# Kernel tuning notes

Hardware: AMD Instinct MI355X
Metric: run time of the kernel (lower is better)

## Reference

```python
import jax, jax.numpy as jnp
import numpy as np

EPS = 1e-5  # BatchNorm2d default eps


def _median_pool3x3(x):
    # x: [B,1,H,W]; 3x3 kernel, stride 1, pad 1 (zero padding, matching F.unfold).
    B, C, H, W = x.shape
    xp = jnp.pad(x, ((0, 0), (0, 0), (1, 1), (1, 1)))
    # Stack the 9 shifted views -> [B,C,H,W,9]; torch.median returns the LOWER
    # median, i.e. sorted index (9-1)//2 = 4 for 9 elements.
    patches = jnp.stack([xp[:, :, i:i + H, j:j + W]
                         for i in range(3) for j in range(3)], axis=-1)
    return jnp.sort(patches, axis=-1)[..., 4]


def _batchnorm_train(x, w, b):
    # BatchNorm2d(1) in training mode: biased variance over (B,H,W) per channel.
    m = jnp.mean(x, axis=(0, 2, 3), keepdims=True)
    v = jnp.mean((x - m) ** 2, axis=(0, 2, 3), keepdims=True)
    return (x - m) * jax.lax.rsqrt(v + EPS) * w.reshape(1, -1, 1, 1) + b.reshape(1, -1, 1, 1)


def _shift_grid_sample(x, xshift, yshift):
    # Faithful to Shift.forward + F.grid_sample(mode='bilinear',
    # padding_mode='zeros', align_corners=False).
    B, C, Nv, Nh = x.shape
    yreg = (jnp.arange(Nv, dtype=x.dtype) - yshift) * 10.0  # [Nv]
    xreg = (jnp.arange(Nh, dtype=x.dtype) - xshift) * 10.0  # [Nh]
    Hv, Wv = Nv * 10.0, Nh * 10.0  # virtual upsampled size used for normalization
    gy = 2.0 * yreg / Hv - 1.0
    gx = 2.0 * xreg / Wv - 1.0
    # unnormalize (align_corners=False): pix = ((g+1)*size - 1)/2
    iy = ((gy + 1.0) * Nv - 1.0) * 0.5  # [Nv]
    ix = ((gx + 1.0) * Nh - 1.0) * 0.5  # [Nh]
    IY, IX = jnp.meshgrid(iy, ix, indexing='ij')  # [Nv,Nh] each

    x0 = jnp.floor(IX); x1 = x0 + 1.0
    y0 = jnp.floor(IY); y1 = y0 + 1.0
    wx1 = IX - x0; wx0 = 1.0 - wx1
    wy1 = IY - y0; wy0 = 1.0 - wy1

    def gather(yc, xc):
        valid = ((yc >= 0) & (yc < Nv) & (xc >= 0) & (xc < Nh)).astype(x.dtype)
        yi = jnp.clip(yc, 0, Nv - 1).astype(jnp.int32)
        xi = jnp.clip(xc, 0, Nh - 1).astype(jnp.int32)
        return x[:, :, yi, xi] * valid  # [B,C,Nv,Nh], zeros outside

    return (gather(y0, x0) * (wy0 * wx0) + gather(y0, x1) * (wy0 * wx1)
            + gather(y1, x0) * (wy1 * wx0) + gather(y1, x1) * (wy1 * wx1))


def setup_inputs() -> dict:
    key = jax.random.key(0)
    ks = jax.random.split(key, 4)
    B, Nv, Nh = 131072, 8, 16
    num_classes, channels = 8, Nv * Nh
    x = jax.random.normal(ks[0], (B, 1, Nv, Nh), dtype=jnp.float32)
    bn_weight = jnp.ones((1,), dtype=jnp.float32)
    bn_bias = jnp.zeros((1,), dtype=jnp.float32)
    xshift = jax.random.uniform(ks[1], (1,), dtype=jnp.float32)
    yshift = jax.random.uniform(ks[2], (1,), dtype=jnp.float32)
    fc_w = jax.random.normal(ks[3], (num_classes, channels), dtype=jnp.float32) / np.sqrt(channels)
    fc_b = jnp.zeros((num_classes,), dtype=jnp.float32)
    return {"x": x, "bn_weight": bn_weight, "bn_bias": bn_bias,
            "xshift": xshift, "yshift": yshift, "fc_w": fc_w, "fc_b": fc_b}


def reference(x, bn_weight, bn_bias, xshift, yshift, fc_w, fc_b):
    h = _median_pool3x3(x)
    h = _batchnorm_train(h, bn_weight, bn_bias)
    h = _shift_grid_sample(h, xshift, yshift)
    h = h.reshape(h.shape[0], -1)  # [B, Nv*Nh]
    return h @ fc_w.T + fc_b  # [B, num_classes]
```

## Files before the change

kernel.cpp:

```cpp
#include <hip/hip_runtime.h>
#include <math.h>

#define NBLK 4096


__device__ __forceinline__ float med3f(float a, float b, float c) {
  return __builtin_amdgcn_fmed3f(a, b, c);
}
__device__ __forceinline__ float min3f(float a, float b, float c) { return fminf(fminf(a, b), c); }
__device__ __forceinline__ float max3f(float a, float b, float c) { return fmaxf(fmaxf(a, b), c); }

__device__ __forceinline__ void fold_weights(int p, const float* __restrict__ fc_w,
                                             float sx, float sy, float* __restrict__ w8) {
  const int y = p >> 4, x = p & 15;
  const int dY = (sy > 1.0f) ? 2 : 1;
  const int dX = (sx > 1.0f) ? 2 : 1;
  const float wy1 = (float)dY - sy, wy0 = 1.0f - wy1;
  const float wx1 = (float)dX - sx, wx0 = 1.0f - wx1;
  const int   iys[2] = { y + dY - 1, y + dY };
  const float wys[2] = { wy1, wy0 };
  const int   jxs[2] = { x + dX - 1, x + dX };
  const float wxs[2] = { wx1, wx0 };
  #pragma unroll
  for (int c = 0; c < 8; ++c) {
    float acc = 0.0f;
    #pragma unroll
    for (int a = 0; a < 2; ++a) {
      if (iys[a] < 0 || iys[a] >= 8) continue;
      #pragma unroll
      for (int b = 0; b < 2; ++b) {
        if (jxs[b] < 0 || jxs[b] >= 16) continue;
        acc += wys[a] * wxs[b] * fc_w[c * 128 + iys[a] * 16 + jxs[b]];
      }
    }
    w8[c] = acc;
  }
}

__global__ __launch_bounds__(256, 2) void k_main(const float* __restrict__ x,
                                                 const float* __restrict__ fcw,
                                                 const float* __restrict__ xs,
                                                 const float* __restrict__ ys,
                                                 float* __restrict__ out,
                                                 float* __restrict__ partial) {
  __shared__ float wlds[8][16][8];
  __shared__ float sred[8];
  const int tid = threadIdx.x;
  const int w = tid >> 6, l = tid & 63;
  const int row = l & 7;
  const int g   = w * 8 + (l >> 3);
  const int img = blockIdx.x * 32 + g;
  const float* __restrict__ xi = x + (size_t)img * 128;

  float mid[16];
  #pragma unroll
  for (int q = 0; q < 4; ++q)
    *(float4*)&mid[q * 4] = *(const float4*)&xi[row * 16 + q * 4];

  const float sx = xs[0] + 0.5f, sy = ys[0] + 0.5f;
  if (tid < 128) {
    float w8[8];
    fold_weights(tid, fcw, sx, sy, w8);
    const int r = tid >> 4, j = tid & 15;
    #pragma unroll
    for (int c = 0; c < 8; ++c) wlds[r][j ^ r][c] = w8[c];
  }
  __syncthreads();

  float up[16], dn[16];
  #pragma unroll
  for (int k = 0; k < 16; ++k) {
    const float u = __shfl_up(mid[k], 1, 16);
    const float d = __shfl_down(mid[k], 1, 16);
    up[k] = (row == 0) ? 0.0f : u;
    dn[k] = (row == 7) ? 0.0f : d;
  }

  #pragma unroll
  for (int k = 0; k < 16; ++k) {
    const float a = up[k], b = mid[k], d = dn[k];
    up[k]  = min3f(a, b, d);
    mid[k] = med3f(a, b, d);
    dn[k]  = max3f(a, b, d);
  }

  float acc[8];
  #pragma unroll
  for (int c = 0; c < 8; ++c) acc[c] = 0.0f;
  float ssum = 0.0f, ssq = 0.0f;

  #pragma unroll
  for (int j = 0; j < 16; ++j) {
    const float mx  = max3f((j == 0)  ? 0.0f : up[j - 1],  up[j],
                            (j == 15) ? 0.0f : up[j + 1]);
    const float md  = med3f((j == 0)  ? 0.0f : mid[j - 1], mid[j],
                            (j == 15) ? 0.0f : mid[j + 1]);
    const float mn  = min3f((j == 0)  ? 0.0f : dn[j - 1],  dn[j],
                            (j == 15) ? 0.0f : dn[j + 1]);
    const float med = med3f(mx, md, mn);
    ssum += med;
    ssq = fmaf(med, med, ssq);
    const float* wp = &wlds[row][j ^ row][0];
    const float4 w0 = *(const float4*)&wp[0];
    const float4 w1 = *(const float4*)&wp[4];
    acc[0] = fmaf(med, w0.x, acc[0]);
    acc[1] = fmaf(med, w0.y, acc[1]);
    acc[2] = fmaf(med, w0.z, acc[2]);
    acc[3] = fmaf(med, w0.w, acc[3]);
    acc[4] = fmaf(med, w1.x, acc[4]);
    acc[5] = fmaf(med, w1.y, acc[5]);
    acc[6] = fmaf(med, w1.z, acc[6]);
    acc[7] = fmaf(med, w1.w, acc[7]);
  }

  const bool b4 = (l & 4) != 0;
  float r4[4];
  #pragma unroll
  for (int j = 0; j < 4; ++j) {
    const float send = b4 ? acc[j] : acc[4 + j];
    const float keep = b4 ? acc[4 + j] : acc[j];
    r4[j] = keep + __shfl_xor(send, 4, 64);
  }
  const bool b2 = (l & 2) != 0;
  float r2[2];
  #pragma unroll
  for (int j = 0; j < 2; ++j) {
    const float send = b2 ? r4[j] : r4[2 + j];
    const float keep = b2 ? r4[2 + j] : r4[j];
    r2[j] = keep + __shfl_xor(send, 2, 64);
  }
  const bool b1 = (l & 1) != 0;
  {
    const float send = b1 ? r2[0] : r2[1];
    const float keep = b1 ? r2[1] : r2[0];
    const float r = keep + __shfl_xor(send, 1, 64);
    out[(size_t)img * 8 + (l & 7)] = r;
  }

  #pragma unroll
  for (int off = 32; off; off >>= 1) {
    ssum += __shfl_xor(ssum, off, 64);
    ssq  += __shfl_xor(ssq,  off, 64);
  }
  if (l == 0) { sred[w] = ssum; sred[4 + w] = ssq; }
  __syncthreads();
  if (tid == 0) partial[2 * blockIdx.x]     = (sred[0] + sred[1]) + (sred[2] + sred[3]);
  if (tid == 1) partial[2 * blockIdx.x + 1] = (sred[4] + sred[5]) + (sred[6] + sred[7]);
}

__global__ __launch_bounds__(256) void k_scale(float* __restrict__ out,
                                               const float* __restrict__ partial,
                                               const float* __restrict__ fcw,
                                               const float* __restrict__ xs,
                                               const float* __restrict__ ys,
                                               const float* __restrict__ fcb,
                                               const float* __restrict__ bnw,
                                               const float* __restrict__ bnb) {
  __shared__ float sred[8];
  __shared__ float wred[4][8];
  __shared__ float fin[2];
  const int tid = threadIdx.x;
  const int w = tid >> 6, l = tid & 63;

  float s = 0.0f, q = 0.0f;
  #pragma unroll
  for (int k = 0; k < 16; ++k) {
    const int idx = tid + 256 * k;
    s += partial[2 * idx];
    q += partial[2 * idx + 1];
  }
  #pragma unroll
  for (int off = 32; off; off >>= 1) {
    s += __shfl_xor(s, off, 64);
    q += __shfl_xor(q, off, 64);
  }

  float v[8];
  if (tid < 128) {
    fold_weights(tid, fcw, xs[0] + 0.5f, ys[0] + 0.5f, v);
  } else {
    #pragma unroll
    for (int c = 0; c < 8; ++c) v[c] = 0.0f;
  }
  #pragma unroll
  for (int c = 0; c < 8; ++c) {
    #pragma unroll
    for (int off = 32; off; off >>= 1) v[c] += __shfl_xor(v[c], off, 64);
  }

  if (l == 0) {
    sred[w] = s; sred[4 + w] = q;
    #pragma unroll
    for (int c = 0; c < 8; ++c) wred[w][c] = v[c];
  }
  __syncthreads();
  if (tid == 0) {
    const float S = (sred[0] + sred[1]) + (sred[2] + sred[3]);
    const float Q = (sred[4] + sred[5]) + (sred[6] + sred[7]);
    const float N = 16777216.0f;
    const float mm = S / N;
    const float vv = Q / N - mm * mm;
    const float a = bnw[0] / sqrtf(vv + 1e-5f);
    fin[0] = a;
    fin[1] = bnb[0] - mm * a;
  }
  __syncthreads();
  const float alpha = fin[0], beta = fin[1];

  float cv[8];
  #pragma unroll
  for (int c = 0; c < 8; ++c) {
    const float wsum = (wred[0][c] + wred[1][c]) + (wred[2][c] + wred[3][c]);
    cv[c] = fmaf(beta, wsum, fcb[c]);
  }
  const float4 cv0 = make_float4(cv[0], cv[1], cv[2], cv[3]);
  const float4 cv1 = make_float4(cv[4], cv[5], cv[6], cv[7]);

  float4* o4 = (float4*)out;
  const int base = (blockIdx.x * 256 + tid) * 4;
  #pragma unroll
  for (int k = 0; k < 4; ++k) {
    const int i = base + k;
    const float4 c = (i & 1) ? cv1 : cv0;
    float4 ov = o4[i];
    ov.x = fmaf(alpha, ov.x, c.x);
    ov.y = fmaf(alpha, ov.y, c.y);
    ov.z = fmaf(alpha, ov.z, c.z);
    ov.w = fmaf(alpha, ov.w, c.w);
    o4[i] = ov;
  }
}

extern "C" void kernel_launch(void* const* d_in, const int* in_sizes, int n_in,
                              void* d_out, int out_size, void* d_ws, size_t ws_size,
                              hipStream_t stream) {
  const float* x   = (const float*)d_in[0];
  const float* bnw = (const float*)d_in[1];
  const float* bnb = (const float*)d_in[2];
  const float* xs  = (const float*)d_in[3];
  const float* ys  = (const float*)d_in[4];
  const float* fcw = (const float*)d_in[5];
  const float* fcb = (const float*)d_in[6];
  float* out = (float*)d_out;
  float* ws  = (float*)d_ws;

  float* partial = ws;

  hipLaunchKernelGGL(k_main,  dim3(NBLK), dim3(256), 0, stream, x, fcw, xs, ys, out, partial);
  hipLaunchKernelGGL(k_scale, dim3(256),  dim3(256), 0, stream, out, partial, fcw, xs, ys, fcb, bnw, bnb);
}
```

Measured before the change: 40.10 us.

## Compute folded FC projection with bf16 MFMA and use DPP row shifts

Replaces the per-thread fp32 FMA dot product and the shuffle-based transpose reduction with a bf16 MFMA 16x16x32 product. Median values are staged through a swizzled LDS tile, and the folded FC weights are stored in LDS as bf16. Only two of the four waves issue the MFMA. The vertical neighbour shuffles are also replaced with DPP row shifts. The intent is to cut ALU, shuffle and LDS-bandwidth cost, at the price of bf16 precision loss in the output and an extra barrier plus LDS round-trip.

```diff
diff --git a/kernel.cpp b/kernel.cpp
--- a/kernel.cpp
+++ b/kernel.cpp
@@ -4,11 +4,26 @@
 #define NBLK 4096
 
 
+typedef __attribute__((ext_vector_type(8))) short bf16x8;
+typedef __attribute__((ext_vector_type(4))) float f32x4;
+
 __device__ __forceinline__ float med3f(float a, float b, float c) {
   return __builtin_amdgcn_fmed3f(a, b, c);
 }
 __device__ __forceinline__ float min3f(float a, float b, float c) { return fminf(fminf(a, b), c); }
 __device__ __forceinline__ float max3f(float a, float b, float c) { return fmaxf(fmaxf(a, b), c); }
+
+__device__ __forceinline__ unsigned bf16rne(float f) {
+  const unsigned b = __float_as_uint(f);
+  return (b + 0x7fffu + ((b >> 16) & 1u)) >> 16;
+}
+
+__device__ __forceinline__ float dpp_up(float v) {
+  return __int_as_float(__builtin_amdgcn_update_dpp(0, __float_as_int(v), 0x111, 0xf, 0xf, true));
+}
+__device__ __forceinline__ float dpp_dn(float v) {
+  return __int_as_float(__builtin_amdgcn_update_dpp(0, __float_as_int(v), 0x101, 0xf, 0xf, true));
+}
 
 __device__ __forceinline__ void fold_weights(int p, const float* __restrict__ fc_w,
                                              float sx, float sy, float* __restrict__ w8) {
@@ -43,35 +58,36 @@
                                                  const float* __restrict__ ys,
                                                  float* __restrict__ out,
                                                  float* __restrict__ partial) {
-  __shared__ float wlds[8][16][8];
+  __shared__ unsigned short wlds[16][128];
+  __shared__ unsigned medl[32][64];
   __shared__ float sred[8];
   const int tid = threadIdx.x;
   const int w = tid >> 6, l = tid & 63;
-  const int row = l & 7;
-  const int g   = w * 8 + (l >> 3);
+  const int g   = tid >> 3;
+  const int row = tid & 7;
   const int img = blockIdx.x * 32 + g;
-  const float* __restrict__ xi = x + (size_t)img * 128;
-
+
+  const float* __restrict__ xr = x + (size_t)img * 128 + row * 16;
   float mid[16];
   #pragma unroll
   for (int q = 0; q < 4; ++q)
-    *(float4*)&mid[q * 4] = *(const float4*)&xi[row * 16 + q * 4];
+    *(float4*)&mid[q * 4] = *(const float4*)&xr[q * 4];
 
   const float sx = xs[0] + 0.5f, sy = ys[0] + 0.5f;
   if (tid < 128) {
     float w8[8];
     fold_weights(tid, fcw, sx, sy, w8);
-    const int r = tid >> 4, j = tid & 15;
-    #pragma unroll
-    for (int c = 0; c < 8; ++c) wlds[r][j ^ r][c] = w8[c];
-  }
-  __syncthreads();
+    #pragma unroll
+    for (int c = 0; c < 8; ++c) wlds[c][tid] = (unsigned short)bf16rne(w8[c]);
+  } else {
+    ((uint4*)&wlds[8][0])[tid - 128] = make_uint4(0, 0, 0, 0);
+  }
 
   float up[16], dn[16];
   #pragma unroll
   for (int k = 0; k < 16; ++k) {
-    const float u = __shfl_up(mid[k], 1, 16);
-    const float d = __shfl_down(mid[k], 1, 16);
+    const float u = dpp_up(mid[k]);
+    const float d = dpp_dn(mid[k]);
     up[k] = (row == 0) ? 0.0f : u;
     dn[k] = (row == 7) ? 0.0f : d;
   }
@@ -84,57 +100,49 @@
     dn[k]  = max3f(a, b, d);
   }
 
-  float acc[8];
-  #pragma unroll
-  for (int c = 0; c < 8; ++c) acc[c] = 0.0f;
+  float med[16];
   float ssum = 0.0f, ssq = 0.0f;
-
   #pragma unroll
   for (int j = 0; j < 16; ++j) {
-    const float mx  = max3f((j == 0)  ? 0.0f : up[j - 1],  up[j],
-                            (j == 15) ? 0.0f : up[j + 1]);
-    const float md  = med3f((j == 0)  ? 0.0f : mid[j - 1], mid[j],
-                            (j == 15) ? 0.0f : mid[j + 1]);
-    const float mn  = min3f((j == 0)  ? 0.0f : dn[j - 1],  dn[j],
-                            (j == 15) ? 0.0f : dn[j + 1]);
-    const float med = med3f(mx, md, mn);
-    ssum += med;
-    ssq = fmaf(med, med, ssq);
-    const float* wp = &wlds[row][j ^ row][0];
-    const float4 w0 = *(const float4*)&wp[0];
-    const float4 w1 = *(const float4*)&wp[4];
-    acc[0] = fmaf(med, w0.x, acc[0]);
-    acc[1] = fmaf(med, w0.y, acc[1]);
-    acc[2] = fmaf(med, w0.z, acc[2]);
-    acc[3] = fmaf(med, w0.w, acc[3]);
-    acc[4] = fmaf(med, w1.x, acc[4]);
-    acc[5] = fmaf(med, w1.y, acc[5]);
-    acc[6] = fmaf(med, w1.z, acc[6]);
-    acc[7] = fmaf(med, w1.w, acc[7]);
-  }
-
-  const bool b4 = (l & 4) != 0;
-  float r4[4];
-  #pragma unroll
-  for (int j = 0; j < 4; ++j) {
-    const float send = b4 ? acc[j] : acc[4 + j];
-    const float keep = b4 ? acc[4 + j] : acc[j];
-    r4[j] = keep + __shfl_xor(send, 4, 64);
-  }
-  const bool b2 = (l & 2) != 0;
-  float r2[2];
-  #pragma unroll
-  for (int j = 0; j < 2; ++j) {
-    const float send = b2 ? r4[j] : r4[2 + j];
-    const float keep = b2 ? r4[2 + j] : r4[j];
-    r2[j] = keep + __shfl_xor(send, 2, 64);
-  }
-  const bool b1 = (l & 1) != 0;
+    const float mx = max3f((j == 0)  ? 0.0f : up[j - 1],  up[j],
+                           (j == 15) ? 0.0f : up[j + 1]);
+    const float md = med3f((j == 0)  ? 0.0f : mid[j - 1], mid[j],
+                           (j == 15) ? 0.0f : mid[j + 1]);
+    const float mn = min3f((j == 0)  ? 0.0f : dn[j - 1],  dn[j],
+                           (j == 15) ? 0.0f : dn[j + 1]);
+    med[j] = med3f(mx, md, mn);
+    ssum += med[j];
+    ssq = fmaf(med[j], med[j], ssq);
+  }
+
   {
-    const float send = b1 ? r2[0] : r2[1];
-    const float keep = b1 ? r2[1] : r2[0];
-    const float r = keep + __shfl_xor(send, 1, 64);
-    out[(size_t)img * 8 + (l & 7)] = r;
+    unsigned u[8];
+    #pragma unroll
+    for (int jj = 0; jj < 8; ++jj)
+      u[jj] = bf16rne(med[2 * jj]) | (bf16rne(med[2 * jj + 1]) << 16);
+    const int rsw = row ^ (g & 7);
+    uint4* mdst = (uint4*)&medl[g][rsw * 8];
+    mdst[0] = make_uint4(u[0], u[1], u[2], u[3]);
+    mdst[1] = make_uint4(u[4], u[5], u[6], u[7]);
+  }
+  __syncthreads();
+
+  if (w < 2) {
+    const int h  = l >> 4;
+    const int li = l & 15;
+    const int ig = w * 16 + li;
+    f32x4 acc = {0.0f, 0.0f, 0.0f, 0.0f};
+    #pragma unroll
+    for (int m = 0; m < 4; ++m) {
+      const int r = 2 * m + (h >> 1);
+      const bf16x8 a = *(const bf16x8*)&wlds[li][m * 32 + h * 8];
+      const bf16x8 b = *(const bf16x8*)&medl[ig][(r ^ (ig & 7)) * 8 + (h & 1) * 4];
+      acc = __builtin_amdgcn_mfma_f32_16x16x32_bf16(a, b, acc, 0, 0, 0);
+    }
+    if (l < 32) {
+      const size_t io = (size_t)(blockIdx.x * 32 + w * 16 + li) * 8 + h * 4;
+      *(float4*)&out[io] = make_float4(acc[0], acc[1], acc[2], acc[3]);
+    }
   }
 
   #pragma unroll
```

New measurement: 35.94 us. -10.4%, faster.
